# Optimization experiments

Measured on AMD Instinct MI355X. Metric: run time of the kernel, lower is better.

## Reference

```python
import jax, jax.numpy as jnp
import numpy as np

N_NODES = 100000
HIDDEN = 512
NUM_GRAPHS = 1024


def setup_inputs() -> dict:
    key = jax.random.key(0)
    k_h, k_b, k_w1, k_w2 = jax.random.split(key, 4)
    s1 = 1.0 / np.sqrt(HIDDEN)
    return {
        "h": jax.random.normal(k_h, (N_NODES, HIDDEN), dtype=jnp.float32),
        "batch_vec": jnp.sort(jax.random.randint(k_b, (N_NODES,), 0, NUM_GRAPHS, dtype=jnp.int32)),
        "W1": jax.random.normal(k_w1, (HIDDEN, HIDDEN), dtype=jnp.float32) * s1,
        "b1": jnp.zeros((HIDDEN,), dtype=jnp.float32),
        "W2": jax.random.normal(k_w2, (HIDDEN, 1), dtype=jnp.float32) * s1,
        "b2": jnp.zeros((1,), dtype=jnp.float32),
    }


def reference(h, batch_vec, W1, b1, W2, b2):
    # gate MLP (Dropout is identity in eval): [N, hidden] -> [N]
    gate = (jax.nn.gelu(h @ W1 + b1, approximate=False) @ W2 + b2)[:, 0]
    # segment softmax over graphs (batch_vec)
    m = jax.ops.segment_max(gate, batch_vec, num_segments=NUM_GRAPHS)
    e = jnp.exp(gate - m[batch_vec])
    denom = jax.ops.segment_sum(e, batch_vec, num_segments=NUM_GRAPHS)
    alpha = e / denom[batch_vec]  # [N]
    # scatter-weighted sum: [num_graphs, hidden]
    return jax.ops.segment_sum(alpha[:, None] * h, batch_vec, num_segments=NUM_GRAPHS)
```

## Files before the change

### kernel.cpp

```cpp
#include <hip/hip_runtime.h>
#include <hip/hip_bf16.h>
#include <float.h>

#define N_NODES 100000
#define HID     512
#define NGRAPH  1024
#define BM      48
#define NBLK    ((N_NODES + BM - 1) / BM)

typedef __bf16 bf16_t;
typedef bf16_t bf16x8 __attribute__((ext_vector_type(8)));
typedef float  f32x4  __attribute__((ext_vector_type(4)));

__device__ __forceinline__ float fast_gelu(float x) {
    const float z = __builtin_fabsf(x) * 0.70710678118654752f;
    const float t = __fdividef(1.0f, __builtin_fmaf(0.3275911f, z, 1.0f));
    float p = __builtin_fmaf(1.061405429f, t, -1.453152027f);
    p = __builtin_fmaf(p, t, 1.421413741f);
    p = __builtin_fmaf(p, t, -0.284496736f);
    p = __builtin_fmaf(p, t, 0.254829592f);
    p *= t;
    const float e    = __expf(-z * z);
    const float erfz = __builtin_fmaf(-p, e, 1.0f);
    const float s    = __builtin_copysignf(erfz, x);
    return 0.5f * x * (1.0f + s);
}

__global__ void __launch_bounds__(256) k_w1t_tiled(const float* __restrict__ w1,
                                                   bf16_t* __restrict__ bt) {
    const int u   = blockIdx.x * 256 + threadIdx.x;
    const int col = u & 511;
    const int g4  = u >> 9;
    const int k0  = g4 * 8;
    bf16x8 v;
    #pragma unroll
    for (int e = 0; e < 8; ++e)
        v[e] = (bf16_t)w1[(size_t)(k0 + e) * HID + col];
    *reinterpret_cast<bf16x8*>(bt + (size_t)u * 8) = v;
}

__global__ void __launch_bounds__(512, 2) k_gemm_gate(const float* __restrict__ h,
                                                      const bf16_t* __restrict__ bt,
                                                      const float* __restrict__ b1,
                                                      const float* __restrict__ w2,
                                                      const float* __restrict__ b2,
                                                      float* __restrict__ gate) {
    __shared__ __align__(16) bf16_t As[BM * HID];
    __shared__ float gp[8][BM];

    const int tid  = threadIdx.x;
    const int lane = tid & 63;
    const int wv   = tid >> 6;
    const int l15  = lane & 15;
    const int l4   = lane >> 4;

    const int brow = blockIdx.x * BM;

    #pragma unroll
    for (int i = 0; i < 6; ++i) {
        const int idx = i * 512 + tid;
        const int row = idx >> 6;
        const int cu  = idx & 63;
        const int grow = brow + row;
        f32x4 s0 = f32x4{0.f, 0.f, 0.f, 0.f}, s1 = s0;
        if (grow < N_NODES) {
            const f32x4* p = reinterpret_cast<const f32x4*>(
                h + (size_t)grow * HID + cu * 8);
            s0 = p[0];
            s1 = p[1];
        }
        bf16x8 v;
        #pragma unroll
        for (int j = 0; j < 4; ++j) { v[j] = (bf16_t)s0[j]; v[4 + j] = (bf16_t)s1[j]; }
        *reinterpret_cast<bf16x8*>(
            (char*)As + row * 1024 + ((cu ^ (row & 7)) * 16)) = v;
    }
    __syncthreads();

    const bf16_t* wbase = bt + ((size_t)l4 * 512 + wv * 64 + l15) * 8;
    const char*   abase = (const char*)As + l15 * 1024;
    const int     sh    = (wv << 1) & 15;
    f32x4 acc[4][3] = {};
    #pragma unroll
    for (int t = 0; t < 16; ++t) {
        const int kt = (t + sh) & 15;
        bf16x8 wfr[4];
        #pragma unroll
        for (int mf = 0; mf < 4; ++mf)
            wfr[mf] = *reinterpret_cast<const bf16x8*>(
                wbase + (size_t)kt * 16384 + mf * 128);
        const int chunkoff = ((kt * 4 + l4) ^ (l15 & 7)) * 16;
        bf16x8 hfr[3];
        #pragma unroll
        for (int nf = 0; nf < 3; ++nf)
            hfr[nf] = *reinterpret_cast<const bf16x8*>(
                abase + nf * 16384 + chunkoff);
        #pragma unroll
        for (int mf = 0; mf < 4; ++mf)
            #pragma unroll
            for (int nf = 0; nf < 3; ++nf)
                acc[mf][nf] = __builtin_amdgcn_mfma_f32_16x16x32_bf16(
                    wfr[mf], hfr[nf], acc[mf][nf], 0, 0, 0);
    }

    float pr[3] = {0.f, 0.f, 0.f};
    #pragma unroll
    for (int mf = 0; mf < 4; ++mf) {
        const int hb = wv * 64 + mf * 16 + l4 * 4;
        const float4 bq = *reinterpret_cast<const float4*>(b1 + hb);
        const float4 wq = *reinterpret_cast<const float4*>(w2 + hb);
        const float bArr[4] = {bq.x, bq.y, bq.z, bq.w};
        const float wArr[4] = {wq.x, wq.y, wq.z, wq.w};
        #pragma unroll
        for (int nf = 0; nf < 3; ++nf) {
            #pragma unroll
            for (int rr = 0; rr < 4; ++rr) {
                const float ge = fast_gelu(acc[mf][nf][rr] + bArr[rr]);
                pr[nf] = fmaf(ge, wArr[rr], pr[nf]);
            }
        }
    }
    #pragma unroll
    for (int nf = 0; nf < 3; ++nf) {
        pr[nf] += __shfl_xor(pr[nf], 16);
        pr[nf] += __shfl_xor(pr[nf], 32);
    }
    if (l4 == 0) {
        #pragma unroll
        for (int nf = 0; nf < 3; ++nf)
            gp[wv][nf * 16 + l15] = pr[nf];
    }
    __syncthreads();
    if (tid < BM) {
        const int grow = brow + tid;
        if (grow < N_NODES) {
            float s = b2[0];
            #pragma unroll
            for (int w = 0; w < 8; ++w) s += gp[w][tid];
            gate[grow] = s;
        }
    }
}

__global__ void __launch_bounds__(256) k_pool(const float* __restrict__ h,
                                              const int* __restrict__ bv,
                                              const float* __restrict__ gate,
                                              float* __restrict__ out) {
    const int g   = blockIdx.x;
    const int tid = threadIdx.x;
    __shared__ int   s_bounds[2];
    __shared__ float s_red[4];
    __shared__ float s_alpha[256];

    if (tid == 0) {
        int lo = 0, hi = N_NODES;
        while (lo < hi) { int mid = (lo + hi) >> 1; if (bv[mid] < g) lo = mid + 1; else hi = mid; }
        s_bounds[0] = lo;
        int lo2 = lo, hi2 = N_NODES;
        while (lo2 < hi2) { int mid = (lo2 + hi2) >> 1; if (bv[mid] < g + 1) lo2 = mid + 1; else hi2 = mid; }
        s_bounds[1] = lo2;
    }
    __syncthreads();
    const int start = s_bounds[0], end = s_bounds[1];

    float2 acc = make_float2(0.f, 0.f);
    if (start < end) {
        const int lane = tid & 63, wv = tid >> 6;
        float lm = -FLT_MAX;
        for (int i = start + tid; i < end; i += 256) lm = fmaxf(lm, gate[i]);
        #pragma unroll
        for (int o = 32; o; o >>= 1) lm = fmaxf(lm, __shfl_xor(lm, o));
        if (lane == 0) s_red[wv] = lm;
        __syncthreads();
        const float m = fmaxf(fmaxf(s_red[0], s_red[1]), fmaxf(s_red[2], s_red[3]));
        __syncthreads();
        float ls = 0.f;
        for (int i = start + tid; i < end; i += 256) ls += expf(gate[i] - m);
        #pragma unroll
        for (int o = 32; o; o >>= 1) ls += __shfl_xor(ls, o);
        if (lane == 0) s_red[wv] = ls;
        __syncthreads();
        const float inv = 1.f / (s_red[0] + s_red[1] + s_red[2] + s_red[3]);
        const float* hcol = h + tid * 2;
        for (int base = start; base < end; base += 256) {
            const int j = base + tid;
            const float av = (j < end) ? expf(gate[j] - m) * inv : 0.f;
            __syncthreads();
            s_alpha[tid] = av;
            __syncthreads();
            const int cnt = min(256, end - base);
            for (int jj = 0; jj < cnt; ++jj) {
                const float a = s_alpha[jj];
                const float2 hv = *reinterpret_cast<const float2*>(
                    hcol + (size_t)(base + jj) * HID);
                acc.x = fmaf(a, hv.x, acc.x);
                acc.y = fmaf(a, hv.y, acc.y);
            }
        }
    }
    *reinterpret_cast<float2*>(out + (size_t)g * HID + tid * 2) = acc;
}

extern "C" void kernel_launch(void* const* d_in, const int* in_sizes, int n_in,
                              void* d_out, int out_size, void* d_ws, size_t ws_size,
                              hipStream_t stream) {
    const float* h  = (const float*)d_in[0];
    const int*   bv = (const int*)d_in[1];
    const float* W1 = (const float*)d_in[2];
    const float* b1 = (const float*)d_in[3];
    const float* W2 = (const float*)d_in[4];
    const float* b2 = (const float*)d_in[5];
    float* out = (float*)d_out;

    char* ws = (char*)d_ws;
    bf16_t* bt   = (bf16_t*)ws;
    float*  gate = (float*)(ws + 524288);

    k_w1t_tiled<<<dim3(128), dim3(256), 0, stream>>>(W1, bt);
    k_gemm_gate<<<dim3(NBLK), dim3(512), 0, stream>>>(h, bt, b1, W2, b2, gate);
    k_pool<<<dim3(NGRAPH), dim3(256), 0, stream>>>(h, bv, gate, out);
}
```

Baseline: 147.5 us.

## Switch gate GEMM to 32x32 MFMA with 1024-thread blocks and prefetched W1 loads

The gate GEMM now uses 32x32x16 bf16 MFMA instructions with a 64-row tile and 16 waves per block, each wave owning 32 hidden columns. W1 fragments are loaded with inline-asm global loads two k-steps ahead, and explicit vmcnt waits overlap global latency with MFMA work. The aim is higher matrix-core efficiency and fewer blocks. In exchange, the hand-written waitcnt scheduling is fragile, and the 1024-thread blocks with a launch-bounds occupancy hint of 4 put pressure on registers.

```diff
diff --git a/kernel.cpp b/kernel.cpp
--- a/kernel.cpp
+++ b/kernel.cpp
@@ -5,12 +5,13 @@
 #define N_NODES 100000
 #define HID     512
 #define NGRAPH  1024
-#define BM      48
+#define BM      64
 #define NBLK    ((N_NODES + BM - 1) / BM)
 
 typedef __bf16 bf16_t;
 typedef bf16_t bf16x8 __attribute__((ext_vector_type(8)));
 typedef float  f32x4  __attribute__((ext_vector_type(4)));
+typedef float  f32x16 __attribute__((ext_vector_type(16)));
 
 __device__ __forceinline__ float fast_gelu(float x) {
     const float z = __builtin_fabsf(x) * 0.70710678118654752f;
@@ -39,26 +40,31 @@
     *reinterpret_cast<bf16x8*>(bt + (size_t)u * 8) = v;
 }
 
-__global__ void __launch_bounds__(512, 2) k_gemm_gate(const float* __restrict__ h,
-                                                      const bf16_t* __restrict__ bt,
-                                                      const float* __restrict__ b1,
-                                                      const float* __restrict__ w2,
-                                                      const float* __restrict__ b2,
-                                                      float* __restrict__ gate) {
+#define BLOAD(dst, elemoff)                                                     \
+    asm volatile("global_load_dwordx4 %0, %1, off"                              \
+                 : "=v"(dst)                                                    \
+                 : "v"((const void*)(wbase + (elemoff))))
+
+__global__ void __launch_bounds__(1024, 4) k_gemm_gate(const float* __restrict__ h,
+                                                       const bf16_t* __restrict__ bt,
+                                                       const float* __restrict__ b1,
+                                                       const float* __restrict__ w2,
+                                                       const float* __restrict__ b2,
+                                                       float* __restrict__ gate) {
     __shared__ __align__(16) bf16_t As[BM * HID];
-    __shared__ float gp[8][BM];
+    __shared__ float gp[16][BM];
 
     const int tid  = threadIdx.x;
     const int lane = tid & 63;
     const int wv   = tid >> 6;
-    const int l15  = lane & 15;
-    const int l4   = lane >> 4;
+    const int l31  = lane & 31;
+    const int l5   = lane >> 5;
 
     const int brow = blockIdx.x * BM;
 
     #pragma unroll
-    for (int i = 0; i < 6; ++i) {
-        const int idx = i * 512 + tid;
+    for (int i = 0; i < 4; ++i) {
+        const int idx = i * 1024 + tid;
         const int row = idx >> 6;
         const int cu  = idx & 63;
         const int grow = brow + row;
@@ -77,58 +83,72 @@
     }
     __syncthreads();
 
-    const bf16_t* wbase = bt + ((size_t)l4 * 512 + wv * 64 + l15) * 8;
-    const char*   abase = (const char*)As + l15 * 1024;
-    const int     sh    = (wv << 1) & 15;
-    f32x4 acc[4][3] = {};
+    const bf16_t* wbase = bt + (size_t)l5 * 4096 + ((size_t)wv * 32 + l31) * 8;
+    const char*   a0 = (const char*)As + l31 * 1024;
+    const char*   a1 = (const char*)As + (32 + l31) * 1024;
+    const int     swz = l31 & 7;
+    const int     sh  = wv;
+    f32x16 acc[2] = {};
+
+    bf16x8 bcA, bcB;
+    bf16x8 bnA, bnB;
+    bf16x8 bmA, bmB;
+    {
+        const size_t o0 = (size_t)(sh & 15) * 16384;
+        BLOAD(bcA, o0); BLOAD(bcB, o0 + 8192);
+        const size_t o1 = (size_t)((sh + 1) & 15) * 16384;
+        BLOAD(bnA, o1); BLOAD(bnB, o1 + 8192);
+    }
     #pragma unroll
     for (int t = 0; t < 16; ++t) {
         const int kt = (t + sh) & 15;
-        bf16x8 wfr[4];
-        #pragma unroll
-        for (int mf = 0; mf < 4; ++mf)
-            wfr[mf] = *reinterpret_cast<const bf16x8*>(
-                wbase + (size_t)kt * 16384 + mf * 128);
-        const int chunkoff = ((kt * 4 + l4) ^ (l15 & 7)) * 16;
-        bf16x8 hfr[3];
-        #pragma unroll
-        for (int nf = 0; nf < 3; ++nf)
-            hfr[nf] = *reinterpret_cast<const bf16x8*>(
-                abase + nf * 16384 + chunkoff);
-        #pragma unroll
-        for (int mf = 0; mf < 4; ++mf)
-            #pragma unroll
-            for (int nf = 0; nf < 3; ++nf)
-                acc[mf][nf] = __builtin_amdgcn_mfma_f32_16x16x32_bf16(
-                    wfr[mf], hfr[nf], acc[mf][nf], 0, 0, 0);
-    }
-
-    float pr[3] = {0.f, 0.f, 0.f};
-    #pragma unroll
-    for (int mf = 0; mf < 4; ++mf) {
-        const int hb = wv * 64 + mf * 16 + l4 * 4;
+        if (t < 14) {
+            const size_t o2 = (size_t)((t + 2 + sh) & 15) * 16384;
+            BLOAD(bmA, o2); BLOAD(bmB, o2 + 8192);
+        }
+        const int c0 = (kt * 4 + l5) ^ swz;
+        const int c1 = (kt * 4 + 2 + l5) ^ swz;
+        bf16x8 h00 = *reinterpret_cast<const bf16x8*>(a0 + c0 * 16);
+        bf16x8 h01 = *reinterpret_cast<const bf16x8*>(a0 + c1 * 16);
+        bf16x8 h10 = *reinterpret_cast<const bf16x8*>(a1 + c0 * 16);
+        bf16x8 h11 = *reinterpret_cast<const bf16x8*>(a1 + c1 * 16);
+        if (t < 14)       asm volatile("s_waitcnt vmcnt(4)" ::: "memory");
+        else if (t == 14) asm volatile("s_waitcnt vmcnt(2)" ::: "memory");
+        else              asm volatile("s_waitcnt vmcnt(0)" ::: "memory");
+        __builtin_amdgcn_sched_barrier(0);
+        acc[0] = __builtin_amdgcn_mfma_f32_32x32x16_bf16(bcA, h00, acc[0], 0, 0, 0);
+        acc[1] = __builtin_amdgcn_mfma_f32_32x32x16_bf16(bcA, h10, acc[1], 0, 0, 0);
+        acc[0] = __builtin_amdgcn_mfma_f32_32x32x16_bf16(bcB, h01, acc[0], 0, 0, 0);
+        acc[1] = __builtin_amdgcn_mfma_f32_32x32x16_bf16(bcB, h11, acc[1], 0, 0, 0);
+        bcA = bnA; bcB = bnB;
+        bnA = bmA; bnB = bmB;
+    }
+
+    float bArr[4][4], wArr[4][4];
+    #pragma unroll
+    for (int rg = 0; rg < 4; ++rg) {
+        const int hb = wv * 32 + 8 * rg + 4 * l5;
         const float4 bq = *reinterpret_cast<const float4*>(b1 + hb);
         const float4 wq = *reinterpret_cast<const float4*>(w2 + hb);
-        const float bArr[4] = {bq.x, bq.y, bq.z, bq.w};
-        const float wArr[4] = {wq.x, wq.y, wq.z, wq.w};
-        #pragma unroll
-        for (int nf = 0; nf < 3; ++nf) {
+        bArr[rg][0] = bq.x; bArr[rg][1] = bq.y; bArr[rg][2] = bq.z; bArr[rg][3] = bq.w;
+        wArr[rg][0] = wq.x; wArr[rg][1] = wq.y; wArr[rg][2] = wq.z; wArr[rg][3] = wq.w;
+    }
+    float pr[2] = {0.f, 0.f};
+    #pragma unroll
+    for (int cb = 0; cb < 2; ++cb) {
+        #pragma unroll
+        for (int rg = 0; rg < 4; ++rg) {
             #pragma unroll
-            for (int rr = 0; rr < 4; ++rr) {
-                const float ge = fast_gelu(acc[mf][nf][rr] + bArr[rr]);
-                pr[nf] = fmaf(ge, wArr[rr], pr[nf]);
+            for (int j = 0; j < 4; ++j) {
+                const float ge = fast_gelu(acc[cb][rg * 4 + j] + bArr[rg][j]);
+                pr[cb] = fmaf(ge, wArr[rg][j], pr[cb]);
             }
         }
-    }
-    #pragma unroll
-    for (int nf = 0; nf < 3; ++nf) {
-        pr[nf] += __shfl_xor(pr[nf], 16);
-        pr[nf] += __shfl_xor(pr[nf], 32);
-    }
-    if (l4 == 0) {
-        #pragma unroll
-        for (int nf = 0; nf < 3; ++nf)
-            gp[wv][nf * 16 + l15] = pr[nf];
+        pr[cb] += __shfl_xor(pr[cb], 32);
+    }
+    if (lane < 32) {
+        gp[wv][l31]      = pr[0];
+        gp[wv][32 + l31] = pr[1];
     }
     __syncthreads();
     if (tid < BM) {
@@ -136,7 +156,7 @@
         if (grow < N_NODES) {
             float s = b2[0];
             #pragma unroll
-            for (int w = 0; w < 8; ++w) s += gp[w][tid];
+            for (int w = 0; w < 16; ++w) s += gp[w][tid];
             gate[grow] = s;
         }
     }
@@ -217,6 +237,6 @@
     float*  gate = (float*)(ws + 524288);
 
     k_w1t_tiled<<<dim3(128), dim3(256), 0, stream>>>(W1, bt);
-    k_gemm_gate<<<dim3(NBLK), dim3(512), 0, stream>>>(h, bt, b1, W2, b2, gate);
+    k_gemm_gate<<<dim3(NBLK), dim3(1024), 0, stream>>>(h, bt, b1, W2, b2, gate);
     k_pool<<<dim3(NGRAPH), dim3(256), 0, stream>>>(h, bv, gate, out);
 }
```

Measured after the change: 154.3 us. 4.7% more time.
